# Kernel optimization log

Measured on AMD Instinct MI355X. Metric: run time of the kernel, lower is better.

Reference implementation:

```python
import jax, jax.numpy as jnp
import numpy as np

N, E, G = 50000, 800000, 512
IN_C, H, EC, L, OUT_C = 16, 128, 16, 4, 1

def _lin(k, fi, fo):
    return jax.random.normal(k, (fi, fo), dtype=jnp.float32) / np.sqrt(fi)

def setup_inputs() -> dict:
    key = jax.random.key(0)
    ks = jax.random.split(key, 32)
    inp = {
        'x_nodes': jax.random.normal(ks[0], (N, IN_C), dtype=jnp.float32),
        'x_edges': jax.random.normal(ks[1], (E, EC), dtype=jnp.float32),
        'edge_index': jax.random.randint(ks[2], (2, E), 0, N),
        'batch': jnp.sort(jax.random.randint(ks[3], (N,), 0, G)),
    }
    # embed_nodes
    inp['emb_w1'] = _lin(ks[4], IN_C, H); inp['emb_b1'] = jnp.zeros((H,), jnp.float32)
    inp['emb_w2'] = _lin(ks[5], H, H);    inp['emb_b2'] = jnp.zeros((H,), jnp.float32)
    # per-layer edge_net / node_net weights, stacked over L
    kk = jax.random.split(ks[6], 4 * L)
    inp['ew1'] = jnp.stack([_lin(kk[i], 2 * H + EC, H) for i in range(L)])
    inp['eb1'] = jnp.zeros((L, H), jnp.float32)
    inp['ew2'] = jnp.stack([_lin(kk[L + i], H, H) for i in range(L)])
    inp['eb2'] = jnp.zeros((L, H), jnp.float32)
    inp['nw1'] = jnp.stack([_lin(kk[2 * L + i], 2 * H, H) for i in range(L)])
    inp['nb1'] = jnp.zeros((L, H), jnp.float32)
    inp['nw2'] = jnp.stack([_lin(kk[3 * L + i], H, H) for i in range(L)])
    inp['nb2'] = jnp.zeros((L, H), jnp.float32)
    # pre_readout / readout
    inp['pr_w1'] = _lin(ks[7], H, H); inp['pr_b1'] = jnp.zeros((H,), jnp.float32)
    inp['pr_w2'] = _lin(ks[8], H, H); inp['pr_b2'] = jnp.zeros((H,), jnp.float32)
    inp['ro_w1'] = _lin(ks[9], H, H); inp['ro_b1'] = jnp.zeros((H,), jnp.float32)
    inp['ro_w2'] = _lin(ks[10], H, OUT_C); inp['ro_b2'] = jnp.zeros((OUT_C,), jnp.float32)
    return inp

def _gnn_forward(x_nodes, x_edges, emb_w1, emb_b1, emb_w2, emb_b2,
                 ew1, eb1, ew2, eb2, nw1, nb1, nw2, nb2,
                 pr_w1, pr_b1, pr_w2, pr_b2, ro_w1, ro_b1, ro_w2, ro_b2,
                 edge_index, batch):
    silu = jax.nn.silu
    sender, receiver = edge_index[0], edge_index[1]
    # embed_nodes
    h = silu(x_nodes @ emb_w1 + emb_b1) @ emb_w2 + emb_b2  # [N, H]
    for l in range(L):
        state = jnp.concatenate((h[sender], h[receiver], x_edges), axis=1)  # [E, 2H+EC]
        msg = silu(silu(state @ ew1[l] + eb1[l]) @ ew2[l] + eb2[l])  # [E, H]
        aggr = jax.ops.segment_sum(msg, receiver, num_segments=N)  # [N, H]
        h = silu(jnp.concatenate((h, aggr), axis=1) @ nw1[l] + nb1[l]) @ nw2[l] + nb2[l]
    h = silu(h @ pr_w1 + pr_b1) @ pr_w2 + pr_b2
    pooled = jax.ops.segment_sum(h, batch, num_segments=G)  # [G, H]
    out = silu(pooled @ ro_w1 + ro_b1) @ ro_w2 + ro_b2  # [G, 1]
    return jnp.squeeze(out)

def reference(x_nodes, x_edges, edge_index, batch,
              emb_w1, emb_b1, emb_w2, emb_b2,
              ew1, eb1, ew2, eb2, nw1, nb1, nw2, nb2,
              pr_w1, pr_b1, pr_w2, pr_b2, ro_w1, ro_b1, ro_w2, ro_b2):
    return _gnn_forward(x_nodes, x_edges, emb_w1, emb_b1, emb_w2, emb_b2,
                        ew1, eb1, ew2, eb2, nw1, nb1, nw2, nb2,
                        pr_w1, pr_b1, pr_w2, pr_b2, ro_w1, ro_b1, ro_w2, ro_b2,
                        edge_index, batch)
```

## Files before the change

kernel.cpp:

```cpp
#include <hip/hip_runtime.h>


typedef short bf16x8 __attribute__((ext_vector_type(8)));
typedef float f32x4 __attribute__((ext_vector_type(4)));

union U8 { bf16x8 v; unsigned short u[8]; unsigned int d[4]; };

__device__ __forceinline__ float bf2f(unsigned short u) {
    union { unsigned int i; float f; } x; x.i = ((unsigned int)u) << 16; return x.f;
}
__device__ __forceinline__ float u32lo2f(unsigned int d) {
    union { unsigned int i; float f; } x; x.i = d << 16; return x.f;
}
__device__ __forceinline__ float u32hi2f(unsigned int d) {
    union { unsigned int i; float f; } x; x.i = d & 0xffff0000u; return x.f;
}
__device__ __forceinline__ unsigned short f2bf(float f) {
    union { float f; unsigned int i; } x; x.f = f;
    unsigned int r = x.i + 0x7FFFu + ((x.i >> 16) & 1u);
    return (unsigned short)(r >> 16);
}
__device__ __forceinline__ unsigned int cvt_pk_bf16(float lo, float hi) {
    unsigned int r;
    asm("v_cvt_pk_bf16_f32 %0, %1, %2" : "=v"(r) : "v"(lo), "v"(hi));
    return r;
}
__device__ __forceinline__ float siluf(float x) { return x / (1.0f + __expf(-x)); }
__device__ __forceinline__ float silu_fast(float x) {
    float e;
    asm("v_exp_f32 %0, %1" : "=v"(e) : "v"(x * -1.44269504089f));
    float r;
    asm("v_rcp_f32 %0, %1" : "=v"(r) : "v"(e + 1.0f));
    return x * r;
}

__global__ void k_hist(const int* __restrict__ recv, int* __restrict__ counts, int E) {
    int i = blockIdx.x * 256 + threadIdx.x;
    if (i < E) atomicAdd(&counts[recv[i]], 1);
}

__global__ __launch_bounds__(1024) void k_scan1(const int* __restrict__ counts,
                                                int* __restrict__ offsets,
                                                int* __restrict__ bsum, int n) {
    __shared__ int buf[1024];
    int i = blockIdx.x * 1024 + threadIdx.x;
    int v = (i < n) ? counts[i] : 0;
    buf[threadIdx.x] = v;
    __syncthreads();
    for (int off = 1; off < 1024; off <<= 1) {
        int t = 0;
        if ((int)threadIdx.x >= off) t = buf[threadIdx.x - off];
        __syncthreads();
        if ((int)threadIdx.x >= off) buf[threadIdx.x] += t;
        __syncthreads();
    }
    if (i < n) offsets[i] = buf[threadIdx.x] - v;
    if (threadIdx.x == 1023) bsum[blockIdx.x] = buf[1023];
}

__global__ void k_scan2(int* __restrict__ bsum, int nb) {
    if (threadIdx.x == 0 && blockIdx.x == 0) {
        int acc = 0;
        for (int b = 0; b < nb; ++b) { int v = bsum[b]; bsum[b] = acc; acc += v; }
    }
}

__global__ __launch_bounds__(1024) void k_scan3(int* __restrict__ offsets,
                                                const int* __restrict__ bsum,
                                                int n, int E) {
    int i = blockIdx.x * 1024 + threadIdx.x;
    if (i < n) offsets[i] += bsum[blockIdx.x];
    if (i == 0) offsets[n] = E;
}

__global__ void k_scatter(const int* __restrict__ send, const int* __restrict__ recv,
                          const int* __restrict__ offsets, int* __restrict__ cursor,
                          int* __restrict__ ss, int* __restrict__ sr,
                          int* __restrict__ perm, int E) {
    int i = blockIdx.x * 256 + threadIdx.x;
    if (i < E) {
        int r = recv[i];
        int pos = offsets[r] + atomicAdd(&cursor[r], 1);
        ss[pos] = send[i];
        sr[pos] = r;
        perm[pos] = i;
    }
}

__global__ void k_permute_xe(const float* __restrict__ xe, const int* __restrict__ perm,
                             unsigned short* __restrict__ out, int E) {
    int t = blockIdx.x * 256 + threadIdx.x;
    if (t < E * 4) {
        int pos = t >> 2, q = t & 3;
        int e = perm[pos];
        float4 v = *(const float4*)(xe + (size_t)e * 16 + q * 4);
        ushort4 o;
        o.x = f2bf(v.x); o.y = f2bf(v.y); o.z = f2bf(v.z); o.w = f2bf(v.w);
        *(ushort4*)(out + (size_t)pos * 16 + q * 4) = o;
    }
}

struct WJob { const float* src; unsigned short* dst; int rows; int perm; };
struct WJobs { WJob j[31]; };

__global__ __launch_bounds__(256) void k_wconv(WJobs jobs) {
    WJob jb = jobs.j[blockIdx.x];
    int n = jb.rows * 128;
    if (jb.perm) {
        for (int i = threadIdx.x; i < n; i += 256) {
            int c = i >> 7, slot = i & 127;
            int feat = (slot >> 3) + 16 * (slot & 7);
            jb.dst[c * 128 + slot] = f2bf(jb.src[feat * 128 + c]);
        }
    } else {
        for (int i = threadIdx.x; i < n; i += 256) {
            int k = i >> 7, c = i & 127;
            jb.dst[c * jb.rows + k] = f2bf(jb.src[i]);
        }
    }
}

__global__ __launch_bounds__(256) void k_embed1(const float* __restrict__ x,
                                                const float* __restrict__ w1,
                                                const float* __restrict__ b1,
                                                unsigned short* __restrict__ out, int N) {
    int idx = blockIdx.x * 256 + threadIdx.x;
    int n = idx >> 6, lane = idx & 63;
    if (n >= N) return;
    const float* xr = x + (size_t)n * 16;
    float xv[16];
#pragma unroll
    for (int k = 0; k < 16; k += 4) {
        float4 v = *(const float4*)(xr + k);
        xv[k] = v.x; xv[k + 1] = v.y; xv[k + 2] = v.z; xv[k + 3] = v.w;
    }
    int c0 = lane * 2;
    float a0 = b1[c0], a1 = b1[c0 + 1];
#pragma unroll
    for (int k = 0; k < 16; ++k) {
        float2 w = *(const float2*)(w1 + k * 128 + c0);
        a0 += xv[k] * w.x; a1 += xv[k] * w.y;
    }
    *(unsigned int*)(out + (size_t)n * 128 + c0) = cvt_pk_bf16(siluf(a0), siluf(a1));
}

__device__ __forceinline__ void load_frags(const unsigned short* __restrict__ A,
                                           int r0, int colb, int kg, int M,
                                           bf16x8 (&Af)[2][4]) {
#pragma unroll
    for (int rf = 0; rf < 2; ++rf) {
        int row = r0 + rf * 16 + colb;
        if (row < M) {
#pragma unroll
            for (int ks = 0; ks < 4; ++ks)
                Af[rf][ks] = *(const bf16x8*)(A + (size_t)row * 128 + ks * 32 + kg * 8);
        } else {
            U8 z;
#pragma unroll
            for (int i = 0; i < 8; ++i) z.u[i] = 0;
#pragma unroll
            for (int ks = 0; ks < 4; ++ks) Af[rf][ks] = z.v;
        }
    }
}

__device__ __forceinline__ void mma_block(const bf16x8 (&Af)[2][4],
                                          const unsigned short* sW,
                                          int colb, int kg, f32x4 (&C)[2][8]) {
#pragma unroll
    for (int ks = 0; ks < 4; ++ks) {
#pragma unroll
        for (int cf = 0; cf < 8; ++cf) {
            bf16x8 B = *(const bf16x8*)(sW + (colb + 16 * cf) * 136 + ks * 32 + kg * 8);
#pragma unroll
            for (int rf = 0; rf < 2; ++rf)
                C[rf][cf] = __builtin_amdgcn_mfma_f32_16x16x32_bf16(Af[rf][ks], B, C[rf][cf], 0, 0, 0);
        }
    }
}

#define STAGE_W(WT) do { __syncthreads(); \
    for (int i_ = tid * 8; i_ < 16384; i_ += 2048) \
        *(bf16x8*)(sW + (i_ >> 7) * 136 + (i_ & 127)) = *(const bf16x8*)((WT) + i_); \
    __syncthreads(); } while (0)

__global__ __launch_bounds__(256, 2) void k_node(
    const unsigned short* __restrict__ A1, const unsigned short* __restrict__ WT1,
    const unsigned short* __restrict__ A2, const unsigned short* __restrict__ WT2,
    const float* __restrict__ b12, int act1,
    unsigned short* __restrict__ out1,
    const unsigned short* __restrict__ WT3, const float* __restrict__ b3,
    unsigned short* __restrict__ out3,
    const unsigned short* __restrict__ WTs, const unsigned short* __restrict__ WTr,
    unsigned short* __restrict__ outPs, unsigned short* __restrict__ outPr,
    int M) {
    __shared__ unsigned short sW[128 * 136];
    __shared__ unsigned short sT[128 * 136];
    int tid = threadIdx.x, lane = tid & 63, w = tid >> 6;
    int r0 = blockIdx.x * 128 + w * 32;
    int colb = lane & 15, kg = lane >> 4;

    f32x4 C[2][8];
#pragma unroll
    for (int cf = 0; cf < 8; ++cf) {
        float bb = b12[colb + 16 * cf];
        C[0][cf] = (f32x4){bb, bb, bb, bb};
        C[1][cf] = C[0][cf];
    }
    bf16x8 Af[2][4];
    STAGE_W(WT1);
    load_frags(A1, r0, colb, kg, M, Af);
    mma_block(Af, sW, colb, kg, C);
    if (WT2) {
        STAGE_W(WT2);
        load_frags(A2, r0, colb, kg, M, Af);
        mma_block(Af, sW, colb, kg, C);
    }
#pragma unroll
    for (int rf = 0; rf < 2; ++rf) {
#pragma unroll
        for (int cf = 0; cf < 8; ++cf) {
            int col = colb + 16 * cf;
#pragma unroll
            for (int j = 0; j < 4; ++j) {
                float v = C[rf][cf][j];
                if (act1) v = siluf(v);
                unsigned short bv = f2bf(v);
                int lrow = w * 32 + rf * 16 + kg * 4 + j;
                sT[lrow * 136 + col] = bv;
                if (out1) {
                    int row = r0 + rf * 16 + kg * 4 + j;
                    if (row < M) out1[(size_t)row * 128 + col] = bv;
                }
            }
        }
    }

    if (WT3) {
        STAGE_W(WT3);
        bf16x8 At[2][4];
#pragma unroll
        for (int rf = 0; rf < 2; ++rf)
#pragma unroll
            for (int ks = 0; ks < 4; ++ks)
                At[rf][ks] = *(const bf16x8*)(sT + (w * 32 + rf * 16 + colb) * 136 + ks * 32 + kg * 8);
#pragma unroll
        for (int cf = 0; cf < 8; ++cf) {
            float bb = b3[colb + 16 * cf];
            C[0][cf] = (f32x4){bb, bb, bb, bb};
            C[1][cf] = C[0][cf];
        }
        mma_block(At, sW, colb, kg, C);
#pragma unroll
        for (int rf = 0; rf < 2; ++rf) {
#pragma unroll
            for (int cf = 0; cf < 8; ++cf) {
                int col = colb + 16 * cf;
#pragma unroll
                for (int j = 0; j < 4; ++j) {
                    unsigned short bv = f2bf(C[rf][cf][j]);
                    int row = r0 + rf * 16 + kg * 4 + j;
                    if (row < M) out3[(size_t)row * 128 + col] = bv;
                    if (WTs) sT[(w * 32 + rf * 16 + kg * 4 + j) * 136 + col] = bv;
                }
            }
        }
    }

    if (WTs) {
        STAGE_W(WTs);
        bf16x8 At[2][4];
#pragma unroll
        for (int rf = 0; rf < 2; ++rf)
#pragma unroll
            for (int ks = 0; ks < 4; ++ks)
                At[rf][ks] = *(const bf16x8*)(sT + (w * 32 + rf * 16 + colb) * 136 + ks * 32 + kg * 8);
#pragma unroll
        for (int rf = 0; rf < 2; ++rf)
#pragma unroll
            for (int cf = 0; cf < 8; ++cf) C[rf][cf] = (f32x4){0.f, 0.f, 0.f, 0.f};
        mma_block(At, sW, colb, kg, C);
#pragma unroll
        for (int rf = 0; rf < 2; ++rf) {
#pragma unroll
            for (int j = 0; j < 4; ++j) {
                int row = r0 + rf * 16 + kg * 4 + j;
                if (row < M) {
                    U8 o;
#pragma unroll
                    for (int q = 0; q < 4; ++q)
                        o.d[q] = cvt_pk_bf16(C[rf][2 * q][j], C[rf][2 * q + 1][j]);
                    *(bf16x8*)(outPs + (size_t)row * 128 + colb * 8) = o.v;
                }
            }
        }
        STAGE_W(WTr);
#pragma unroll
        for (int rf = 0; rf < 2; ++rf)
#pragma unroll
            for (int cf = 0; cf < 8; ++cf) C[rf][cf] = (f32x4){0.f, 0.f, 0.f, 0.f};
        mma_block(At, sW, colb, kg, C);
#pragma unroll
        for (int rf = 0; rf < 2; ++rf) {
#pragma unroll
            for (int j = 0; j < 4; ++j) {
                int row = r0 + rf * 16 + kg * 4 + j;
                if (row < M) {
                    U8 o;
#pragma unroll
                    for (int q = 0; q < 4; ++q)
                        o.d[q] = cvt_pk_bf16(C[rf][2 * q][j], C[rf][2 * q + 1][j]);
                    *(bf16x8*)(outPr + (size_t)row * 128 + colb * 8) = o.v;
                }
            }
        }
    }
}

__global__ __launch_bounds__(256, 3) void k_msg(
    const unsigned short* __restrict__ Ps, const unsigned short* __restrict__ Pr,
    const unsigned short* __restrict__ xes,
    const int* __restrict__ ss, const int* __restrict__ sr,
    const unsigned short* __restrict__ WeT, const float* __restrict__ b1,
    const unsigned short* __restrict__ W2T, const float* __restrict__ b2,
    unsigned short* __restrict__ aggr, float* __restrict__ pbuf,
    int* __restrict__ pid, int ntiles) {
    __shared__ unsigned short sW2[128 * 136];
    __shared__ unsigned short sT[64 * 136];
    __shared__ float sB2[128];
    __shared__ int sRid[64];
    int tid = threadIdx.x, lane = tid & 63, w = tid >> 6;
    int colb = lane & 15, kg = lane >> 4;
    int R0 = w * 16, rb = R0 + kg * 4;

    for (int i = tid * 8; i < 16384; i += 2048)
        *(bf16x8*)(sW2 + (i >> 7) * 136 + (i & 127)) = *(const bf16x8*)(W2T + i);
    if (tid < 128) sB2[tid] = b2[tid];
    bf16x8 WeB[8];
#pragma unroll
    for (int cf = 0; cf < 8; ++cf) {
        if (kg < 2) WeB[cf] = *(const bf16x8*)(WeT + (colb + 16 * cf) * 16 + kg * 8);
        else { U8 z; for (int i = 0; i < 8; ++i) z.u[i] = 0; WeB[cf] = z.v; }
    }
    float b1v[8];
#pragma unroll
    for (int cf = 0; cf < 8; ++cf) b1v[cf] = b1[colb + 16 * cf];
    int s = lane * 2;
    int c0 = (s >> 3) + 16 * (s & 7);
    __syncthreads();

    int stride = gridDim.x;
    int t = blockIdx.x;
    U8 zz; for (int i = 0; i < 8; ++i) zz.u[i] = 0;
    bf16x8 Axe = zz.v;
    U8 gp[8];
    int4 s4 = *(const int4*)(ss + (t << 6) + rb);
    int4 r4 = *(const int4*)(sr + (t << 6) + rb);

#define ISSUE_GATHER(S4, R4, TT) do { \
        gp[0].v = *(const bf16x8*)(Ps + (size_t)(S4).x * 128 + colb * 8); \
        gp[1].v = *(const bf16x8*)(Ps + (size_t)(S4).y * 128 + colb * 8); \
        gp[2].v = *(const bf16x8*)(Ps + (size_t)(S4).z * 128 + colb * 8); \
        gp[3].v = *(const bf16x8*)(Ps + (size_t)(S4).w * 128 + colb * 8); \
        gp[4].v = *(const bf16x8*)(Pr + (size_t)(R4).x * 128 + colb * 8); \
        gp[5].v = *(const bf16x8*)(Pr + (size_t)(R4).y * 128 + colb * 8); \
        gp[6].v = *(const bf16x8*)(Pr + (size_t)(R4).z * 128 + colb * 8); \
        gp[7].v = *(const bf16x8*)(Pr + (size_t)(R4).w * 128 + colb * 8); \
        if (kg < 2) Axe = *(const bf16x8*)(xes + (size_t)(((TT) << 6) + R0 + colb) * 16 + kg * 8); \
    } while (0)

    ISSUE_GATHER(s4, r4, t);
    for (;;) {
        if (colb == 0) {
            sRid[rb] = r4.x; sRid[rb + 1] = r4.y; sRid[rb + 2] = r4.z; sRid[rb + 3] = r4.w;
        }
        int tn = t + stride;
        bool more = tn < ntiles;
        int4 s4n, r4n;
        if (more) {
            s4n = *(const int4*)(ss + (tn << 6) + rb);
            r4n = *(const int4*)(sr + (tn << 6) + rb);
        }
        f32x4 xc[8];
#pragma unroll
        for (int cf = 0; cf < 8; ++cf) {
            f32x4 bb = (f32x4){b1v[cf], b1v[cf], b1v[cf], b1v[cf]};
            xc[cf] = __builtin_amdgcn_mfma_f32_16x16x32_bf16(Axe, WeB[cf], bb, 0, 0, 0);
        }
#pragma unroll
        for (int j = 0; j < 4; ++j) {
            U8 o;
#pragma unroll
            for (int q = 0; q < 4; ++q) {
                float v0 = u32lo2f(gp[j].d[q]) + u32lo2f(gp[4 + j].d[q]) + xc[2 * q][j];
                float v1 = u32hi2f(gp[j].d[q]) + u32hi2f(gp[4 + j].d[q]) + xc[2 * q + 1][j];
                o.d[q] = cvt_pk_bf16(silu_fast(v0), silu_fast(v1));
            }
            *(bf16x8*)(sT + (rb + j) * 136 + colb * 8) = o.v;
        }
        int tcur = t;
        if (more) ISSUE_GATHER(s4n, r4n, tn);
        asm volatile("s_waitcnt lgkmcnt(0)" ::: "memory");
        __builtin_amdgcn_sched_barrier(0);
        bf16x8 Bt[4];
#pragma unroll
        for (int ks = 0; ks < 4; ++ks)
            Bt[ks] = *(const bf16x8*)(sT + (R0 + colb) * 136 + ks * 32 + kg * 8);
        f32x4 m[8];
#pragma unroll
        for (int acf = 0; acf < 8; ++acf)
            m[acf] = *(const f32x4*)(sB2 + acf * 16 + kg * 4);
#pragma unroll
        for (int ks = 0; ks < 4; ++ks) {
#pragma unroll
            for (int acf = 0; acf < 8; ++acf) {
                bf16x8 Aw = *(const bf16x8*)(sW2 + (16 * acf + colb) * 136 + ks * 32 + kg * 8);
                m[acf] = __builtin_amdgcn_mfma_f32_16x16x32_bf16(Aw, Bt[ks], m[acf], 0, 0, 0);
            }
        }
#pragma unroll
        for (int j = 0; j < 4; ++j) {
            U8 o;
#pragma unroll
            for (int q = 0; q < 4; ++q)
                o.d[q] = cvt_pk_bf16(silu_fast(m[2 * q][j]), silu_fast(m[2 * q + 1][j]));
            *(bf16x8*)(sT + (R0 + colb) * 136 + (kg * 4 + j) * 8) = o.v;
        }
        asm volatile("s_waitcnt lgkmcnt(0)" ::: "memory");
        __builtin_amdgcn_sched_barrier(0);
        {
            int run = tcur * 4 + w;
            float a0 = 0.f, a1 = 0.f;
            int prev = sRid[R0];
            bool first = true;
            for (int i = 0; i < 16; ++i) {
                int rid = sRid[R0 + i];
                if (rid != prev) {
                    if (first) {
                        float2 vv; vv.x = a0; vv.y = a1;
                        *(float2*)(pbuf + (size_t)(2 * run) * 128 + s) = vv;
                        if (lane == 0) pid[2 * run] = prev;
                        first = false;
                    } else {
                        aggr[(size_t)prev * 128 + c0] = f2bf(a0);
                        aggr[(size_t)prev * 128 + c0 + 16] = f2bf(a1);
                    }
                    a0 = 0.f; a1 = 0.f; prev = rid;
                }
                unsigned int v = *(const unsigned int*)(sT + (R0 + i) * 136 + s);
                a0 += u32lo2f(v); a1 += u32hi2f(v);
            }
            float2 vv; vv.x = a0; vv.y = a1;
            if (first) {
                *(float2*)(pbuf + (size_t)(2 * run) * 128 + s) = vv;
                if (lane == 0) { pid[2 * run] = prev; pid[2 * run + 1] = -1; }
            } else {
                *(float2*)(pbuf + (size_t)(2 * run + 1) * 128 + s) = vv;
                if (lane == 0) pid[2 * run + 1] = prev;
            }
        }
        if (!more) break;
        s4 = s4n; r4 = r4n; t = tn;
    }
#undef ISSUE_GATHER
}

__global__ __launch_bounds__(256) void k_fix(
    const float* __restrict__ pbuf, const int* __restrict__ pid,
    const int* __restrict__ offsets, unsigned short* __restrict__ aggr, int N) {
    int gw = (blockIdx.x * 256 + threadIdx.x) >> 6;
    int lane = threadIdx.x & 63;
    int nw = (gridDim.x * 256) >> 6;
    int s = lane * 2;
    int c0 = (s >> 3) + 16 * (s & 7);
    for (int n = gw; n < N; n += nw) {
        int o0 = offsets[n], o1 = offsets[n + 1];
        if (o0 >= o1) continue;
        int t0 = o0 >> 4, t1 = (o1 - 1) >> 4;
        if (t0 == t1 && o0 > (t0 << 4) && o1 <= (t0 << 4) + 15) continue;
        float a0 = 0.f, a1 = 0.f;
        for (int tt = t0; tt <= t1; ++tt) {
            if (pid[2 * tt] == n) {
                float2 v = *(const float2*)(pbuf + (size_t)(2 * tt) * 128 + s);
                a0 += v.x; a1 += v.y;
            }
            if (pid[2 * tt + 1] == n) {
                float2 v = *(const float2*)(pbuf + (size_t)(2 * tt + 1) * 128 + s);
                a0 += v.x; a1 += v.y;
            }
        }
        aggr[(size_t)n * 128 + c0] = f2bf(a0);
        aggr[(size_t)n * 128 + c0 + 16] = f2bf(a1);
    }
}

__device__ __forceinline__ int lowerb(const int* a, int n, int v) {
    int lo = 0, hi = n;
    while (lo < hi) { int mid = (lo + hi) >> 1; if (a[mid] < v) lo = mid + 1; else hi = mid; }
    return lo;
}

__global__ __launch_bounds__(128) void k_pool(const unsigned short* __restrict__ hpr,
                                              const int* __restrict__ batch,
                                              float* __restrict__ pooled, int N) {
    __shared__ int s_lo, s_hi;
    int g = blockIdx.x;
    if (threadIdx.x == 0) { s_lo = lowerb(batch, N, g); s_hi = lowerb(batch, N, g + 1); }
    __syncthreads();
    int c = threadIdx.x;
    float acc = 0.f;
    for (int r = s_lo; r < s_hi; ++r) acc += bf2f(hpr[(size_t)r * 128 + c]);
    pooled[(size_t)g * 128 + c] = acc;
}

__global__ __launch_bounds__(128) void k_readout(const float* __restrict__ pooled,
                                                 const float* __restrict__ w1,
                                                 const float* __restrict__ b1,
                                                 const float* __restrict__ w2,
                                                 const float* __restrict__ b2,
                                                 float* __restrict__ out) {
    __shared__ float sp[128];
    __shared__ float sred[2];
    int g = blockIdx.x, t = threadIdx.x;
    sp[t] = pooled[(size_t)g * 128 + t];
    __syncthreads();
    float acc = b1[t];
    for (int k = 0; k < 128; ++k) acc += sp[k] * w1[k * 128 + t];
    float val = siluf(acc) * w2[t];
#pragma unroll
    for (int off = 32; off; off >>= 1) val += __shfl_down(val, off);
    if ((t & 63) == 0) sred[t >> 6] = val;
    __syncthreads();
    if (t == 0) out[g] = sred[0] + sred[1] + b2[0];
}

extern "C" void kernel_launch(void* const* d_in, const int* in_sizes, int n_in,
                              void* d_out, int out_size, void* d_ws, size_t ws_size,
                              hipStream_t stream) {
    const float* x_nodes = (const float*)d_in[0];
    const float* x_edges = (const float*)d_in[1];
    const int* edge_index = (const int*)d_in[2];
    const int* batch = (const int*)d_in[3];
    const float* emb_w1 = (const float*)d_in[4];
    const float* emb_b1 = (const float*)d_in[5];
    const float* emb_w2 = (const float*)d_in[6];
    const float* emb_b2 = (const float*)d_in[7];
    const float* ew1 = (const float*)d_in[8];
    const float* eb1 = (const float*)d_in[9];
    const float* ew2 = (const float*)d_in[10];
    const float* eb2 = (const float*)d_in[11];
    const float* nw1 = (const float*)d_in[12];
    const float* nb1 = (const float*)d_in[13];
    const float* nw2 = (const float*)d_in[14];
    const float* nb2 = (const float*)d_in[15];
    const float* pr_w1 = (const float*)d_in[16];
    const float* pr_b1 = (const float*)d_in[17];
    const float* pr_w2 = (const float*)d_in[18];
    const float* pr_b2 = (const float*)d_in[19];
    const float* ro_w1 = (const float*)d_in[20];
    const float* ro_b1 = (const float*)d_in[21];
    const float* ro_w2 = (const float*)d_in[22];
    const float* ro_b2 = (const float*)d_in[23];

    const int N = in_sizes[0] / 16;
    const int E = in_sizes[1] / 16;
    const int G = 512;
    const int L = 4;
    const int nruns = E >> 4;
    const int ntiles = E >> 6;

    char* p = (char*)d_ws;
    auto alloc = [&](size_t bytes) {
        void* r = p;
        p += (bytes + 255) & ~(size_t)255;
        return r;
    };
    int* counts = (int*)alloc((size_t)N * 4);
    int* cursor = (int*)alloc((size_t)N * 4);
    int* offsets = (int*)alloc((size_t)(N + 1) * 4);
    int* bsum = (int*)alloc((size_t)256 * 4);
    int* ss = (int*)alloc((size_t)E * 4);
    int* sr = (int*)alloc((size_t)E * 4);
    int* perm = (int*)alloc((size_t)E * 4);
    unsigned short* xes = (unsigned short*)alloc((size_t)E * 16 * 2);
    unsigned short* h = (unsigned short*)alloc((size_t)N * 128 * 2);
    unsigned short* t0buf = (unsigned short*)alloc((size_t)N * 128 * 2);
    unsigned short* Ps = (unsigned short*)alloc((size_t)N * 128 * 2);
    unsigned short* Pr = (unsigned short*)alloc((size_t)N * 128 * 2);
    unsigned short* aggr = (unsigned short*)alloc((size_t)N * 128 * 2);
    unsigned short* hpr = (unsigned short*)alloc((size_t)N * 128 * 2);
    float* pooled = (float*)alloc((size_t)G * 128 * 4);
    float* pbuf = (float*)alloc((size_t)nruns * 2 * 128 * 4);
    int* pid = (int*)alloc((size_t)nruns * 2 * 4);

    const size_t WSZ = 128 * 128;
    unsigned short* wt_emb2 = (unsigned short*)alloc(WSZ * 2);
    unsigned short *wtWs[4], *wtWr[4], *wtWe[4], *wtW2[4], *wtN1a[4], *wtN1b[4], *wtN2[4];
    for (int l = 0; l < L; ++l) {
        wtWs[l] = (unsigned short*)alloc(WSZ * 2);
        wtWr[l] = (unsigned short*)alloc(WSZ * 2);
        wtWe[l] = (unsigned short*)alloc((size_t)16 * 128 * 2);
        wtW2[l] = (unsigned short*)alloc(WSZ * 2);
        wtN1a[l] = (unsigned short*)alloc(WSZ * 2);
        wtN1b[l] = (unsigned short*)alloc(WSZ * 2);
        wtN2[l] = (unsigned short*)alloc(WSZ * 2);
    }
    unsigned short* wt_pr1 = (unsigned short*)alloc(WSZ * 2);
    unsigned short* wt_pr2 = (unsigned short*)alloc(WSZ * 2);

    const int* send = edge_index;
    const int* recv = edge_index + E;

    hipMemsetAsync(counts, 0, (size_t)N * 4, stream);
    hipMemsetAsync(cursor, 0, (size_t)N * 4, stream);
    hipMemsetAsync(aggr, 0, (size_t)N * 128 * 2, stream);
    k_hist<<<(E + 255) / 256, 256, 0, stream>>>(recv, counts, E);
    int nb = (N + 1023) / 1024;
    k_scan1<<<nb, 1024, 0, stream>>>(counts, offsets, bsum, N);
    k_scan2<<<1, 64, 0, stream>>>(bsum, nb);
    k_scan3<<<nb, 1024, 0, stream>>>(offsets, bsum, N, E);
    k_scatter<<<(E + 255) / 256, 256, 0, stream>>>(send, recv, offsets, cursor, ss, sr, perm, E);
    k_permute_xe<<<(E * 4 + 255) / 256, 256, 0, stream>>>(x_edges, perm, xes, E);

    WJobs jobs;
    int nj = 0;
    auto addj = [&](const float* s, unsigned short* d, int rows, int pm) {
        jobs.j[nj].src = s; jobs.j[nj].dst = d; jobs.j[nj].rows = rows; jobs.j[nj].perm = pm; ++nj;
    };
    addj(emb_w2, wt_emb2, 128, 0);
    for (int l = 0; l < L; ++l) {
        const float* ew1_l = ew1 + (size_t)l * 272 * 128;
        addj(ew1_l, wtWs[l], 128, 0);
        addj(ew1_l + 128 * 128, wtWr[l], 128, 0);
        addj(ew1_l + 256 * 128, wtWe[l], 16, 0);
        addj(ew2 + (size_t)l * WSZ, wtW2[l], 128, 1);
        const float* nw1_l = nw1 + (size_t)l * 256 * 128;
        addj(nw1_l, wtN1a[l], 128, 0);
        addj(nw1_l + 128 * 128, wtN1b[l], 128, 0);
        addj(nw2 + (size_t)l * WSZ, wtN2[l], 128, 0);
    }
    addj(pr_w1, wt_pr1, 128, 0);
    addj(pr_w2, wt_pr2, 128, 0);
    k_wconv<<<nj, 256, 0, stream>>>(jobs);

    int gb = (N + 127) / 128;
    k_embed1<<<(N * 64 + 255) / 256, 256, 0, stream>>>(x_nodes, emb_w1, emb_b1, t0buf, N);
    k_node<<<gb, 256, 0, stream>>>(t0buf, wt_emb2, nullptr, nullptr, emb_b2, 0,
                                   h, nullptr, nullptr, nullptr,
                                   wtWs[0], wtWr[0], Ps, Pr, N);

    int mg = ntiles < 2048 ? ntiles : 2048;
    for (int l = 0; l < L; ++l) {
        k_msg<<<mg, 256, 0, stream>>>(Ps, Pr, xes, ss, sr, wtWe[l], eb1 + l * 128,
                                      wtW2[l], eb2 + l * 128, aggr, pbuf, pid, ntiles);
        k_fix<<<1024, 256, 0, stream>>>(pbuf, pid, offsets, aggr, N);
        k_node<<<gb, 256, 0, stream>>>(h, wtN1a[l], aggr, wtN1b[l], nb1 + l * 128, 1,
                                       nullptr, wtN2[l], nb2 + l * 128, h,
                                       (l < L - 1) ? wtWs[l + 1] : nullptr,
                                       (l < L - 1) ? wtWr[l + 1] : nullptr,
                                       Ps, Pr, N);
    }

    k_node<<<gb, 256, 0, stream>>>(h, wt_pr1, nullptr, nullptr, pr_b1, 1,
                                   nullptr, wt_pr2, pr_b2, hpr,
                                   nullptr, nullptr, nullptr, nullptr, N);
    k_pool<<<G, 128, 0, stream>>>(hpr, batch, pooled, N);
    k_readout<<<G, 128, 0, stream>>>(pooled, ro_w1, ro_b1, ro_w2, ro_b2, (float*)d_out);
}
```

Baseline: 930.0 us.

## Shrink node GEMM tile to 64 rows, prefetch A frags, packed adds in message kernel

Changes k_node from 128-row to 64-row tiles (one 16-row fragment per wave), halving the sT buffer and raising launch bounds to 3 blocks per CU, so more blocks run and occupancy rises. Both A operand fragments are now loaded before weight staging so the global loads overlap with the LDS fill. In k_msg, bf16 pair accumulations use v_pk_add_f32, and the persistent grid size becomes ntiles/5 instead of min(ntiles,2048). The smaller tiles mean each block reuses the staged weights over fewer rows, so weight staging traffic per row doubles.

```diff
diff --git a/kernel.cpp b/kernel.cpp
--- a/kernel.cpp
+++ b/kernel.cpp
@@ -3,6 +3,7 @@
 
 typedef short bf16x8 __attribute__((ext_vector_type(8)));
 typedef float f32x4 __attribute__((ext_vector_type(4)));
+typedef float f32x2 __attribute__((ext_vector_type(2)));
 
 union U8 { bf16x8 v; unsigned short u[8]; unsigned int d[4]; };
 
@@ -24,6 +25,16 @@
     unsigned int r;
     asm("v_cvt_pk_bf16_f32 %0, %1, %2" : "=v"(r) : "v"(lo), "v"(hi));
     return r;
+}
+__device__ __forceinline__ f32x2 pk_add(f32x2 a, f32x2 b) {
+    f32x2 r;
+    asm("v_pk_add_f32 %0, %1, %2" : "=v"(r) : "v"(a), "v"(b));
+    return r;
+}
+__device__ __forceinline__ f32x2 up2(unsigned int d) {
+    union { unsigned int i; float f; } lo, hi;
+    lo.i = d << 16; hi.i = d & 0xffff0000u;
+    f32x2 r; r[0] = lo.f; r[1] = hi.f; return r;
 }
 __device__ __forceinline__ float siluf(float x) { return x / (1.0f + __expf(-x)); }
 __device__ __forceinline__ float silu_fast(float x) {
@@ -144,37 +155,32 @@
     *(unsigned int*)(out + (size_t)n * 128 + c0) = cvt_pk_bf16(siluf(a0), siluf(a1));
 }
 
-__device__ __forceinline__ void load_frags(const unsigned short* __restrict__ A,
-                                           int r0, int colb, int kg, int M,
-                                           bf16x8 (&Af)[2][4]) {
-#pragma unroll
-    for (int rf = 0; rf < 2; ++rf) {
-        int row = r0 + rf * 16 + colb;
-        if (row < M) {
-#pragma unroll
-            for (int ks = 0; ks < 4; ++ks)
-                Af[rf][ks] = *(const bf16x8*)(A + (size_t)row * 128 + ks * 32 + kg * 8);
-        } else {
-            U8 z;
-#pragma unroll
-            for (int i = 0; i < 8; ++i) z.u[i] = 0;
-#pragma unroll
-            for (int ks = 0; ks < 4; ++ks) Af[rf][ks] = z.v;
-        }
-    }
-}
-
-__device__ __forceinline__ void mma_block(const bf16x8 (&Af)[2][4],
-                                          const unsigned short* sW,
-                                          int colb, int kg, f32x4 (&C)[2][8]) {
+__device__ __forceinline__ void load_frags64(const unsigned short* __restrict__ A,
+                                             int r0, int colb, int kg, int M,
+                                             bf16x8 (&Af)[4]) {
+    int row = r0 + colb;
+    if (row < M) {
+#pragma unroll
+        for (int ks = 0; ks < 4; ++ks)
+            Af[ks] = *(const bf16x8*)(A + (size_t)row * 128 + ks * 32 + kg * 8);
+    } else {
+        U8 z;
+#pragma unroll
+        for (int i = 0; i < 8; ++i) z.u[i] = 0;
+#pragma unroll
+        for (int ks = 0; ks < 4; ++ks) Af[ks] = z.v;
+    }
+}
+
+__device__ __forceinline__ void mma64(const bf16x8 (&Af)[4],
+                                      const unsigned short* sW,
+                                      int colb, int kg, f32x4 (&C)[8]) {
 #pragma unroll
     for (int ks = 0; ks < 4; ++ks) {
 #pragma unroll
         for (int cf = 0; cf < 8; ++cf) {
             bf16x8 B = *(const bf16x8*)(sW + (colb + 16 * cf) * 136 + ks * 32 + kg * 8);
-#pragma unroll
-            for (int rf = 0; rf < 2; ++rf)
-                C[rf][cf] = __builtin_amdgcn_mfma_f32_16x16x32_bf16(Af[rf][ks], B, C[rf][cf], 0, 0, 0);
+            C[cf] = __builtin_amdgcn_mfma_f32_16x16x32_bf16(Af[ks], B, C[cf], 0, 0, 0);
         }
     }
 }
@@ -184,7 +190,7 @@
         *(bf16x8*)(sW + (i_ >> 7) * 136 + (i_ & 127)) = *(const bf16x8*)((WT) + i_); \
     __syncthreads(); } while (0)
 
-__global__ __launch_bounds__(256, 2) void k_node(
+__global__ __launch_bounds__(256, 3) void k_node(
     const unsigned short* __restrict__ A1, const unsigned short* __restrict__ WT1,
     const unsigned short* __restrict__ A2, const unsigned short* __restrict__ WT2,
     const float* __restrict__ b12, int act1,
@@ -195,123 +201,100 @@
     unsigned short* __restrict__ outPs, unsigned short* __restrict__ outPr,
     int M) {
     __shared__ unsigned short sW[128 * 136];
-    __shared__ unsigned short sT[128 * 136];
+    __shared__ unsigned short sT[64 * 136];
     int tid = threadIdx.x, lane = tid & 63, w = tid >> 6;
-    int r0 = blockIdx.x * 128 + w * 32;
+    int r0 = blockIdx.x * 64 + w * 16;
     int colb = lane & 15, kg = lane >> 4;
 
-    f32x4 C[2][8];
+    f32x4 C[8];
 #pragma unroll
     for (int cf = 0; cf < 8; ++cf) {
         float bb = b12[colb + 16 * cf];
-        C[0][cf] = (f32x4){bb, bb, bb, bb};
-        C[1][cf] = C[0][cf];
-    }
-    bf16x8 Af[2][4];
+        C[cf] = (f32x4){bb, bb, bb, bb};
+    }
+    bf16x8 Af[4], Af2[4];
+    load_frags64(A1, r0, colb, kg, M, Af);
+    if (WT2) load_frags64(A2, r0, colb, kg, M, Af2);
     STAGE_W(WT1);
-    load_frags(A1, r0, colb, kg, M, Af);
-    mma_block(Af, sW, colb, kg, C);
+    mma64(Af, sW, colb, kg, C);
     if (WT2) {
         STAGE_W(WT2);
-        load_frags(A2, r0, colb, kg, M, Af);
-        mma_block(Af, sW, colb, kg, C);
-    }
-#pragma unroll
-    for (int rf = 0; rf < 2; ++rf) {
+        mma64(Af2, sW, colb, kg, C);
+    }
+#pragma unroll
+    for (int cf = 0; cf < 8; ++cf) {
+        int col = colb + 16 * cf;
+#pragma unroll
+        for (int j = 0; j < 4; ++j) {
+            float v = C[cf][j];
+            if (act1) v = siluf(v);
+            unsigned short bv = f2bf(v);
+            sT[(w * 16 + kg * 4 + j) * 136 + col] = bv;
+            if (out1) {
+                int row = r0 + kg * 4 + j;
+                if (row < M) out1[(size_t)row * 128 + col] = bv;
+            }
+        }
+    }
+
+    if (WT3) {
+        STAGE_W(WT3);
+        bf16x8 At[4];
+#pragma unroll
+        for (int ks = 0; ks < 4; ++ks)
+            At[ks] = *(const bf16x8*)(sT + (w * 16 + colb) * 136 + ks * 32 + kg * 8);
+#pragma unroll
+        for (int cf = 0; cf < 8; ++cf) {
+            float bb = b3[colb + 16 * cf];
+            C[cf] = (f32x4){bb, bb, bb, bb};
+        }
+        mma64(At, sW, colb, kg, C);
 #pragma unroll
         for (int cf = 0; cf < 8; ++cf) {
             int col = colb + 16 * cf;
 #pragma unroll
             for (int j = 0; j < 4; ++j) {
-                float v = C[rf][cf][j];
-                if (act1) v = siluf(v);
-                unsigned short bv = f2bf(v);
-                int lrow = w * 32 + rf * 16 + kg * 4 + j;
-                sT[lrow * 136 + col] = bv;
-                if (out1) {
-                    int row = r0 + rf * 16 + kg * 4 + j;
-                    if (row < M) out1[(size_t)row * 128 + col] = bv;
-                }
-            }
-        }
-    }
-
-    if (WT3) {
-        STAGE_W(WT3);
-        bf16x8 At[2][4];
-#pragma unroll
-        for (int rf = 0; rf < 2; ++rf)
-#pragma unroll
-            for (int ks = 0; ks < 4; ++ks)
-                At[rf][ks] = *(const bf16x8*)(sT + (w * 32 + rf * 16 + colb) * 136 + ks * 32 + kg * 8);
-#pragma unroll
-        for (int cf = 0; cf < 8; ++cf) {
-            float bb = b3[colb + 16 * cf];
-            C[0][cf] = (f32x4){bb, bb, bb, bb};
-            C[1][cf] = C[0][cf];
-        }
-        mma_block(At, sW, colb, kg, C);
-#pragma unroll
-        for (int rf = 0; rf < 2; ++rf) {
-#pragma unroll
-            for (int cf = 0; cf < 8; ++cf) {
-                int col = colb + 16 * cf;
-#pragma unroll
-                for (int j = 0; j < 4; ++j) {
-                    unsigned short bv = f2bf(C[rf][cf][j]);
-                    int row = r0 + rf * 16 + kg * 4 + j;
-                    if (row < M) out3[(size_t)row * 128 + col] = bv;
-                    if (WTs) sT[(w * 32 + rf * 16 + kg * 4 + j) * 136 + col] = bv;
-                }
+                unsigned short bv = f2bf(C[cf][j]);
+                int row = r0 + kg * 4 + j;
+                if (row < M) out3[(size_t)row * 128 + col] = bv;
+                if (WTs) sT[(w * 16 + kg * 4 + j) * 136 + col] = bv;
             }
         }
     }
 
     if (WTs) {
         STAGE_W(WTs);
-        bf16x8 At[2][4];
-#pragma unroll
-        for (int rf = 0; rf < 2; ++rf)
-#pragma unroll
-            for (int ks = 0; ks < 4; ++ks)
-                At[rf][ks] = *(const bf16x8*)(sT + (w * 32 + rf * 16 + colb) * 136 + ks * 32 + kg * 8);
-#pragma unroll
-        for (int rf = 0; rf < 2; ++rf)
-#pragma unroll
-            for (int cf = 0; cf < 8; ++cf) C[rf][cf] = (f32x4){0.f, 0.f, 0.f, 0.f};
-        mma_block(At, sW, colb, kg, C);
-#pragma unroll
-        for (int rf = 0; rf < 2; ++rf) {
-#pragma unroll
-            for (int j = 0; j < 4; ++j) {
-                int row = r0 + rf * 16 + kg * 4 + j;
-                if (row < M) {
-                    U8 o;
-#pragma unroll
-                    for (int q = 0; q < 4; ++q)
-                        o.d[q] = cvt_pk_bf16(C[rf][2 * q][j], C[rf][2 * q + 1][j]);
-                    *(bf16x8*)(outPs + (size_t)row * 128 + colb * 8) = o.v;
-                }
+        bf16x8 At[4];
+#pragma unroll
+        for (int ks = 0; ks < 4; ++ks)
+            At[ks] = *(const bf16x8*)(sT + (w * 16 + colb) * 136 + ks * 32 + kg * 8);
+#pragma unroll
+        for (int cf = 0; cf < 8; ++cf) C[cf] = (f32x4){0.f, 0.f, 0.f, 0.f};
+        mma64(At, sW, colb, kg, C);
+#pragma unroll
+        for (int j = 0; j < 4; ++j) {
+            int row = r0 + kg * 4 + j;
+            if (row < M) {
+                U8 o;
+#pragma unroll
+                for (int q = 0; q < 4; ++q)
+                    o.d[q] = cvt_pk_bf16(C[2 * q][j], C[2 * q + 1][j]);
+                *(bf16x8*)(outPs + (size_t)row * 128 + colb * 8) = o.v;
             }
         }
         STAGE_W(WTr);
 #pragma unroll
-        for (int rf = 0; rf < 2; ++rf)
-#pragma unroll
-            for (int cf = 0; cf < 8; ++cf) C[rf][cf] = (f32x4){0.f, 0.f, 0.f, 0.f};
-        mma_block(At, sW, colb, kg, C);
-#pragma unroll
-        for (int rf = 0; rf < 2; ++rf) {
-#pragma unroll
-            for (int j = 0; j < 4; ++j) {
-                int row = r0 + rf * 16 + kg * 4 + j;
-                if (row < M) {
-                    U8 o;
-#pragma unroll
-                    for (int q = 0; q < 4; ++q)
-                        o.d[q] = cvt_pk_bf16(C[rf][2 * q][j], C[rf][2 * q + 1][j]);
-                    *(bf16x8*)(outPr + (size_t)row * 128 + colb * 8) = o.v;
-                }
+        for (int cf = 0; cf < 8; ++cf) C[cf] = (f32x4){0.f, 0.f, 0.f, 0.f};
+        mma64(At, sW, colb, kg, C);
+#pragma unroll
+        for (int j = 0; j < 4; ++j) {
+            int row = r0 + kg * 4 + j;
+            if (row < M) {
+                U8 o;
+#pragma unroll
+                for (int q = 0; q < 4; ++q)
+                    o.d[q] = cvt_pk_bf16(C[2 * q][j], C[2 * q + 1][j]);
+                *(bf16x8*)(outPr + (size_t)row * 128 + colb * 8) = o.v;
             }
         }
     }
@@ -392,8 +375,9 @@
             U8 o;
 #pragma unroll
             for (int q = 0; q < 4; ++q) {
-                float v0 = u32lo2f(gp[j].d[q]) + u32lo2f(gp[4 + j].d[q]) + xc[2 * q][j];
-                float v1 = u32hi2f(gp[j].d[q]) + u32hi2f(gp[4 + j].d[q]) + xc[2 * q + 1][j];
+                f32x2 tp = pk_add(up2(gp[j].d[q]), up2(gp[4 + j].d[q]));
+                float v0 = tp[0] + xc[2 * q][j];
+                float v1 = tp[1] + xc[2 * q + 1][j];
                 o.d[q] = cvt_pk_bf16(silu_fast(v0), silu_fast(v1));
             }
             *(bf16x8*)(sT + (rb + j) * 136 + colb * 8) = o.v;
@@ -430,27 +414,27 @@
         __builtin_amdgcn_sched_barrier(0);
         {
             int run = tcur * 4 + w;
-            float a0 = 0.f, a1 = 0.f;
+            f32x2 acc = (f32x2){0.f, 0.f};
             int prev = sRid[R0];
             bool first = true;
             for (int i = 0; i < 16; ++i) {
                 int rid = sRid[R0 + i];
                 if (rid != prev) {
                     if (first) {
-                        float2 vv; vv.x = a0; vv.y = a1;
+                        float2 vv; vv.x = acc[0]; vv.y = acc[1];
                         *(float2*)(pbuf + (size_t)(2 * run) * 128 + s) = vv;
                         if (lane == 0) pid[2 * run] = prev;
                         first = false;
                     } else {
-                        aggr[(size_t)prev * 128 + c0] = f2bf(a0);
-                        aggr[(size_t)prev * 128 + c0 + 16] = f2bf(a1);
+                        aggr[(size_t)prev * 128 + c0] = f2bf(acc[0]);
+                        aggr[(size_t)prev * 128 + c0 + 16] = f2bf(acc[1]);
                     }
-                    a0 = 0.f; a1 = 0.f; prev = rid;
+                    acc = (f32x2){0.f, 0.f}; prev = rid;
                 }
                 unsigned int v = *(const unsigned int*)(sT + (R0 + i) * 136 + s);
-                a0 += u32lo2f(v); a1 += u32hi2f(v);
-            }
-            float2 vv; vv.x = a0; vv.y = a1;
+                acc = pk_add(acc, up2(v));
+            }
+            float2 vv; vv.x = acc[0]; vv.y = acc[1];
             if (first) {
                 *(float2*)(pbuf + (size_t)(2 * run) * 128 + s) = vv;
                 if (lane == 0) { pid[2 * run] = prev; pid[2 * run + 1] = -1; }
@@ -643,13 +627,15 @@
     addj(pr_w2, wt_pr2, 128, 0);
     k_wconv<<<nj, 256, 0, stream>>>(jobs);
 
-    int gb = (N + 127) / 128;
+    int gb = (N + 63) / 64;
     k_embed1<<<(N * 64 + 255) / 256, 256, 0, stream>>>(x_nodes, emb_w1, emb_b1, t0buf, N);
     k_node<<<gb, 256, 0, stream>>>(t0buf, wt_emb2, nullptr, nullptr, emb_b2, 0,
                                    h, nullptr, nullptr, nullptr,
                                    wtWs[0], wtWr[0], Ps, Pr, N);
 
-    int mg = ntiles < 2048 ? ntiles : 2048;
+    int mg = (ntiles + 4) / 5;
+    if (mg < 1) mg = 1;
+    if (mg > ntiles) mg = ntiles;
     for (int l = 0; l < L; ++l) {
         k_msg<<<mg, 256, 0, stream>>>(Ps, Pr, xes, ss, sr, wtWe[l], eb1 + l * 128,
                                       wtW2[l], eb2 + l * 128, aggr, pbuf, pid, ntiles);
```

Result: slower. 1.004 ms (+8.0%).

## Prefetch next weight matrix into registers while current MMA block runs

Applied to the files above, without the earlier changes.

Splits weight staging into a global-to-register load and a register-to-LDS write. The next stage's weights are loaded into registers before the current matrix multiply, so global memory latency overlaps with MFMA work. The second A operand is also loaded early. This adds 8 bf16x8 registers plus a second fragment set, which raises register pressure under launch_bounds(256,2) and could cause spills or lower occupancy.

```diff
diff --git a/kernel.cpp b/kernel.cpp
--- a/kernel.cpp
+++ b/kernel.cpp
@@ -179,9 +179,18 @@
     }
 }
 
-#define STAGE_W(WT) do { __syncthreads(); \
-    for (int i_ = tid * 8; i_ < 16384; i_ += 2048) \
-        *(bf16x8*)(sW + (i_ >> 7) * 136 + (i_ & 127)) = *(const bf16x8*)((WT) + i_); \
+#define WLOAD(WT) do { \
+    _Pragma("unroll") \
+    for (int k_ = 0; k_ < 8; ++k_) \
+        wreg[k_] = *(const bf16x8*)((WT) + tid * 8 + k_ * 2048); \
+} while (0)
+
+#define WWRITE() do { __syncthreads(); \
+    _Pragma("unroll") \
+    for (int k_ = 0; k_ < 8; ++k_) { \
+        int i_ = tid * 8 + k_ * 2048; \
+        *(bf16x8*)(sW + (i_ >> 7) * 136 + (i_ & 127)) = wreg[k_]; \
+    } \
     __syncthreads(); } while (0)
 
 __global__ __launch_bounds__(256, 2) void k_node(
@@ -199,6 +208,7 @@
     int tid = threadIdx.x, lane = tid & 63, w = tid >> 6;
     int r0 = blockIdx.x * 128 + w * 32;
     int colb = lane & 15, kg = lane >> 4;
+    bf16x8 wreg[8];
 
     f32x4 C[2][8];
 #pragma unroll
@@ -207,14 +217,19 @@
         C[0][cf] = (f32x4){bb, bb, bb, bb};
         C[1][cf] = C[0][cf];
     }
-    bf16x8 Af[2][4];
-    STAGE_W(WT1);
+    bf16x8 Af[2][4], Af2[2][4];
+    WLOAD(WT1);
     load_frags(A1, r0, colb, kg, M, Af);
+    if (WT2) load_frags(A2, r0, colb, kg, M, Af2);
+    WWRITE();
+    if (WT2) WLOAD(WT2);
     mma_block(Af, sW, colb, kg, C);
     if (WT2) {
-        STAGE_W(WT2);
-        load_frags(A2, r0, colb, kg, M, Af);
-        mma_block(Af, sW, colb, kg, C);
+        WWRITE();
+        if (WT3) WLOAD(WT3);
+        mma_block(Af2, sW, colb, kg, C);
+    } else if (WT3) {
+        WLOAD(WT3);
     }
 #pragma unroll
     for (int rf = 0; rf < 2; ++rf) {
@@ -237,7 +252,8 @@
     }
 
     if (WT3) {
-        STAGE_W(WT3);
+        WWRITE();
+        if (WTs) WLOAD(WTs);
         bf16x8 At[2][4];
 #pragma unroll
         for (int rf = 0; rf < 2; ++rf)
@@ -265,10 +281,13 @@
                 }
             }
         }
+    } else if (WTs) {
+        WLOAD(WTs);
     }
 
     if (WTs) {
-        STAGE_W(WTs);
+        WWRITE();
+        WLOAD(WTr);
         bf16x8 At[2][4];
 #pragma unroll
         for (int rf = 0; rf < 2; ++rf)
@@ -294,7 +313,7 @@
                 }
             }
         }
-        STAGE_W(WTr);
+        WWRITE();
 #pragma unroll
         for (int rf = 0; rf < 2; ++rf)
 #pragma unroll
```

Measured after the change: 921.8 us. Within noise of the previous version (-0.9%).
